# Kernel optimization log

Hardware: AMD Instinct MI355X
Metric: run time of the kernel (lower is better)

The kernel has to match this reference:

```python
import jax, jax.numpy as jnp
import numpy as np

B, S, H, E, V = 4, 256, 1024, 1024, 50257
PAD = 0
DOM = 0.9   # skipLayersDominance
EPS = 1e-5  # LayerNorm eps (torch default)


def setup_inputs() -> dict:
    key = jax.random.key(0)
    ks = jax.random.split(key, 6)
    emb = jax.random.normal(ks[0], (V, E), jnp.float32) * 0.02
    emb = emb.at[PAD].set(0.0)  # padding_idx row zeroed like nn.Embedding
    labels = jax.random.randint(ks[1], (B, S), 0, V)
    W_in = jax.random.normal(ks[2], (E, H), jnp.float32) * (1.0 / np.sqrt(E))
    b_in = jnp.zeros((H,), jnp.float32)
    # Conv1d(2H, H, kernel_size=1, groups=H) weight -> [H, 2] (per-head pair mix)
    W_sani = jax.random.normal(ks[3], (H, 2), jnp.float32) * (1.0 / np.sqrt(2.0))
    b_sani = jnp.zeros((H,), jnp.float32)
    ln_w = jnp.ones((H,), jnp.float32)
    ln_b = jnp.zeros((H,), jnp.float32)
    W_out = jax.random.normal(ks[4], (H, E), jnp.float32) * (1.0 / np.sqrt(H))
    b_out = jnp.zeros((E,), jnp.float32)
    return dict(labels=labels, emb=emb, W_in=W_in, b_in=b_in, W_sani=W_sani,
                b_sani=b_sani, ln_w=ln_w, ln_b=ln_b, W_out=W_out, b_out=b_out)


def _layernorm(x, w, b):
    mu = x.mean(-1, keepdims=True)
    var = x.var(-1, keepdims=True)
    return (x - mu) * jax.lax.rsqrt(var + EPS) * w + b


def _forward(labels, emb, W_in, b_in, W_sani, b_sani, ln_w, ln_b, W_out, b_out):
    x = emb[labels]                                # [B,S,E] inputsEmbeddings
    h = jax.nn.relu(x @ W_in + b_in)               # [B,S,H] inputState
    pos = jnp.arange(S)

    def step(hidden, L):
        # positions <= L are replaced by blank (zeros) per the torch cat logic
        mask = (pos > L)[None, :, None]
        shifted = jnp.concatenate([jnp.zeros_like(hidden[:, :1]), hidden[:, :-1]], axis=1)
        prev = jnp.where(mask, shifted, 0.0)       # hidden[t-1] for t>L else 0
        curr = jnp.where(mask, hidden, 0.0)        # hidden[t]   for t>L else 0
        # torch stack(dim=1)+reshape(B, 2H, 1) == concat(prev, curr) on features;
        # grouped conv (groups=H, 2 ch/group, k=1): out[g] = W[g,0]*cat[2g] + W[g,1]*cat[2g+1] + b[g]
        pair = jnp.concatenate([prev, curr], axis=-1).reshape(B, S, H, 2)
        out = jax.nn.relu(jnp.einsum('bshc,hc->bsh', pair, W_sani) + b_sani)
        out = out * (1.0 - DOM) + hidden           # skipLayers: + sequentialInputState
        out = _layernorm(out, ln_w, ln_b)           # skipLayersNorm
        return out, None

    h, _ = jax.lax.scan(jax.checkpoint(step), h, jnp.arange(S))
    y = jax.nn.relu(h @ W_out + b_out)             # [B,S,E]
    # torch CrossEntropyLoss with float (soft) targets: classes along dim=1 (S)
    logp = jax.nn.log_softmax(y, axis=1)
    loss = -(x * logp).sum(axis=1).mean()
    return loss


def reference(labels, emb, W_in, b_in, W_sani, b_sani, ln_w, ln_b, W_out, b_out):
    return _forward(labels, emb, W_in, b_in, W_sani, b_sani, ln_w, ln_b, W_out, b_out)
```

## Files before the change

### kernel.cpp

```cpp
#include <hip/hip_runtime.h>
#include <cstdint>

#define H_DIM 1024
#define S_LEN 256
#define NBLK_SCAN 128
#define GDEPTH 16
#define DOMC ((float)(1.0 - 0.9))
#define EPS_LN 1e-5f

typedef float v2f __attribute__((ext_vector_type(2)));

template <int CTRL, int RMASK, bool BC>
__device__ __forceinline__ float dpp_term(float x) {
    return __int_as_float(__builtin_amdgcn_update_dpp(
        0, __float_as_int(x), CTRL, RMASK, 0xf, BC));
}
__device__ __forceinline__ float wave_reduce_sum(float x) {
    x += dpp_term<0x111, 0xf, true>(x);
    x += dpp_term<0x112, 0xf, true>(x);
    x += dpp_term<0x114, 0xf, true>(x);
    x += dpp_term<0x118, 0xf, true>(x);
    x += dpp_term<0x142, 0xa, false>(x);
    x += dpp_term<0x143, 0xc, false>(x);
    return __int_as_float(__builtin_amdgcn_readlane(__float_as_int(x), 63));
}

__device__ __forceinline__ int llc_load_int(const int* p) {
    int v;
    asm volatile("global_load_dword %0, %1, off sc0 sc1\n\ts_waitcnt vmcnt(0)"
                 : "=v"(v) : "v"(p) : "memory");
    return v;
}
__device__ __forceinline__ void llc_store_int(int* p, int v) {
    asm volatile("global_store_dword %0, %1, off sc0 sc1" :: "v"(p), "v"(v)
                 : "memory");
}
__device__ __forceinline__ void llc_store_row_nowait(float* base, const float* h) {
    asm volatile(
        "global_store_dword %16, %0, off sc0 sc1\n\t"
        "global_store_dword %16, %1, off offset:256 sc0 sc1\n\t"
        "global_store_dword %16, %2, off offset:512 sc0 sc1\n\t"
        "global_store_dword %16, %3, off offset:768 sc0 sc1\n\t"
        "global_store_dword %16, %4, off offset:1024 sc0 sc1\n\t"
        "global_store_dword %16, %5, off offset:1280 sc0 sc1\n\t"
        "global_store_dword %16, %6, off offset:1536 sc0 sc1\n\t"
        "global_store_dword %16, %7, off offset:1792 sc0 sc1\n\t"
        "global_store_dword %16, %8, off offset:2048 sc0 sc1\n\t"
        "global_store_dword %16, %9, off offset:2304 sc0 sc1\n\t"
        "global_store_dword %16, %10, off offset:2560 sc0 sc1\n\t"
        "global_store_dword %16, %11, off offset:2816 sc0 sc1\n\t"
        "global_store_dword %16, %12, off offset:3072 sc0 sc1\n\t"
        "global_store_dword %16, %13, off offset:3328 sc0 sc1\n\t"
        "global_store_dword %16, %14, off offset:3584 sc0 sc1\n\t"
        "global_store_dword %16, %15, off offset:3840 sc0 sc1"
        :: "v"(h[0]), "v"(h[1]), "v"(h[2]), "v"(h[3]),
           "v"(h[4]), "v"(h[5]), "v"(h[6]), "v"(h[7]),
           "v"(h[8]), "v"(h[9]), "v"(h[10]), "v"(h[11]),
           "v"(h[12]), "v"(h[13]), "v"(h[14]), "v"(h[15]), "v"(base)
        : "memory");
}
__device__ __forceinline__ void llc_publish_lag2(float* dbase, int* flagp,
                                                 int flagval, const float* h) {
    asm volatile(
        "s_waitcnt vmcnt(16)\n\t"
        "global_store_dword %17, %18, off sc0 sc1\n\t"
        "global_store_dword %16, %0, off sc0 sc1\n\t"
        "global_store_dword %16, %1, off offset:256 sc0 sc1\n\t"
        "global_store_dword %16, %2, off offset:512 sc0 sc1\n\t"
        "global_store_dword %16, %3, off offset:768 sc0 sc1\n\t"
        "global_store_dword %16, %4, off offset:1024 sc0 sc1\n\t"
        "global_store_dword %16, %5, off offset:1280 sc0 sc1\n\t"
        "global_store_dword %16, %6, off offset:1536 sc0 sc1\n\t"
        "global_store_dword %16, %7, off offset:1792 sc0 sc1\n\t"
        "global_store_dword %16, %8, off offset:2048 sc0 sc1\n\t"
        "global_store_dword %16, %9, off offset:2304 sc0 sc1\n\t"
        "global_store_dword %16, %10, off offset:2560 sc0 sc1\n\t"
        "global_store_dword %16, %11, off offset:2816 sc0 sc1\n\t"
        "global_store_dword %16, %12, off offset:3072 sc0 sc1\n\t"
        "global_store_dword %16, %13, off offset:3328 sc0 sc1\n\t"
        "global_store_dword %16, %14, off offset:3584 sc0 sc1\n\t"
        "global_store_dword %16, %15, off offset:3840 sc0 sc1"
        :: "v"(h[0]), "v"(h[1]), "v"(h[2]), "v"(h[3]),
           "v"(h[4]), "v"(h[5]), "v"(h[6]), "v"(h[7]),
           "v"(h[8]), "v"(h[9]), "v"(h[10]), "v"(h[11]),
           "v"(h[12]), "v"(h[13]), "v"(h[14]), "v"(h[15]),
           "v"(dbase), "v"(flagp), "v"(flagval)
        : "memory");
}
__device__ __forceinline__ void llc_release(int* flagp, int flagval) {
    asm volatile("s_waitcnt vmcnt(0)\n\t"
                 "global_store_dword %0, %1, off sc0 sc1"
                 :: "v"(flagp), "v"(flagval) : "memory");
}

__device__ __forceinline__ void dma_slot(const float* gslot, float* stg, int l) {
#pragma unroll
    for (int c = 0; c < 4; ++c)
        __builtin_amdgcn_global_load_lds(
            (const __attribute__((address_space(1))) uint32_t*)(gslot + c * 256 + l * 4),
            (__attribute__((address_space(3))) uint32_t*)(stg + c * 256),
            16, 0, 0x11);
}

__device__ __forceinline__ void make_pairs(const float* hv, v2f* c7, int l) {
    const int s0 = (2 * l) & 63, s1 = (2 * l + 1) & 63;
    const bool hi = (l >= 32);
#pragma unroll
    for (int j = 0; j < 8; ++j) {
        float x0 = __shfl(hv[2 * j], s0, 64);
        float x1 = __shfl(hv[2 * j + 1], s0, 64);
        float y0 = __shfl(hv[2 * j], s1, 64);
        float y1 = __shfl(hv[2 * j + 1], s1, 64);
        c7[j].x = hi ? x1 : x0;
        c7[j].y = hi ? y1 : y0;
    }
}

template <bool GATHER>
__global__ __launch_bounds__(256) void gemm_relu_kernel(
    const float* __restrict__ A, const int* __restrict__ labels,
    const float* __restrict__ emb, const float* __restrict__ W,
    const float* __restrict__ bias, float* __restrict__ out)
{
    __shared__ float As[16][68];
    __shared__ float Bs[16][64];
    __shared__ int   lab[64];

    const int tid = threadIdx.x;
    const int bx = blockIdx.x & 15;
    const int by = blockIdx.x >> 4;
    const int m0 = by * 64, n0 = bx * 64;

    if (GATHER && tid < 64) lab[tid] = labels[m0 + tid];
    __syncthreads();

    const int tx = tid & 15, ty = tid >> 4;
    const int mload = tid >> 2;
    const int kq    = (tid & 3) * 4;
    const int kb    = tid >> 4;
    const int nb    = (tid & 15) * 4;

    const float* aBase;
    if (GATHER) aBase = emb + (size_t)lab[mload] * 1024 + kq;
    else        aBase = A   + (size_t)(m0 + mload) * 1024 + kq;
    const float* bBase = W + (size_t)kb * 1024 + n0 + nb;

    float4 a_pre = *(const float4*)aBase;
    float4 b_pre = *(const float4*)bBase;

    float acc[4][4] = {};

    for (int k0 = 0; k0 < 1024; k0 += 16) {
        As[kq + 0][mload] = a_pre.x;
        As[kq + 1][mload] = a_pre.y;
        As[kq + 2][mload] = a_pre.z;
        As[kq + 3][mload] = a_pre.w;
        *(float4*)&Bs[kb][nb] = b_pre;
        __syncthreads();

        if (k0 + 16 < 1024) {
            a_pre = *(const float4*)(aBase + k0 + 16);
            b_pre = *(const float4*)(bBase + (size_t)(k0 + 16) * 1024);
        }

#pragma unroll
        for (int kk = 0; kk < 16; ++kk) {
            float a_[4];
#pragma unroll
            for (int i = 0; i < 4; ++i) a_[i] = As[kk][ty * 4 + i];
            float4 bv = *(const float4*)&Bs[kk][tx * 4];
            float b_[4] = {bv.x, bv.y, bv.z, bv.w};
#pragma unroll
            for (int i = 0; i < 4; ++i)
#pragma unroll
                for (int j = 0; j < 4; ++j)
                    acc[i][j] = fmaf(a_[i], b_[j], acc[i][j]);
        }
        __syncthreads();
    }

    float bias4[4];
#pragma unroll
    for (int j = 0; j < 4; ++j) bias4[j] = bias[n0 + tx * 4 + j];
#pragma unroll
    for (int i = 0; i < 4; ++i) {
        float4 o;
        o.x = fmaxf(acc[i][0] + bias4[0], 0.f);
        o.y = fmaxf(acc[i][1] + bias4[1], 0.f);
        o.z = fmaxf(acc[i][2] + bias4[2], 0.f);
        o.w = fmaxf(acc[i][3] + bias4[3], 0.f);
        *(float4*)&out[(size_t)(m0 + ty * 4 + i) * 1024 + n0 + tx * 4] = o;
    }
}

__global__ __launch_bounds__(256) void scan_init_kernel(
    int* __restrict__ prodG, int* __restrict__ consG)
{
    const int tid = threadIdx.x;
    if (tid < NBLK_SCAN) { prodG[tid * 32] = -2; consG[tid * 32] = -2; }
}

__global__ __launch_bounds__(512, 1) void scan_kernel(
    const float* __restrict__ h0, float* __restrict__ hf,
    const float* __restrict__ Wsani, const float* __restrict__ bsani,
    const float* __restrict__ lnw, const float* __restrict__ lnb,
    float* __restrict__ gbuf, int* __restrict__ prodG, int* __restrict__ consG)
{
    __shared__ float ring[7][2][H_DIM];
    __shared__ float stg[H_DIM];
    __shared__ int prodL[8], consL[8];

    const int tid = threadIdx.x, w = tid >> 6, l = tid & 63;
    const int Bb = blockIdx.x;
    const int b = Bb >> 5, p = Bb & 31;
    const int t = 8 * p + w;
    const int row = b * S_LEN + t;
    const bool hasR = (p < 31);
    const int leftB = Bb - 1, rightB = Bb + 1;

    float w0c[16], w1c[16], bsc[16], lwc[16], lbc[16], hv[16];
#pragma unroll
    for (int i = 0; i < 16; ++i) {
        int h = l + 64 * i;
        w0c[i] = Wsani[2 * h]; w1c[i] = Wsani[2 * h + 1];
        bsc[i] = bsani[h]; lwc[i] = lnw[h]; lbc[i] = lnb[h];
        hv[i] = h0[(size_t)row * H_DIM + h];
    }

    if (tid < 8) { prodL[tid] = -2; consL[tid] = -2; }
    __syncthreads();

    v2f c7[8];
    if (w < 7) {
#pragma unroll
        for (int i = 0; i < 16; ++i) ring[w][1][l + 64 * i] = hv[i];
        __threadfence_block();
        if (l == 0) ((volatile int*)prodL)[w] = -1;
    } else {
        if (hasR)
            llc_store_row_nowait(
                gbuf + ((size_t)Bb * GDEPTH + (GDEPTH - 1)) * H_DIM + l, hv);
        make_pairs(hv, c7, l);
    }

    const float inv1024 = 1.f / 1024.f;
    int F = -2, pfL = -3, consCache = -2;
    float vv[16];

    for (int L = 0; L < S_LEN; ++L) {
        const bool active = (L < t);
        if (active) {
            v2f pv[8], cv[8];
            if (w == 0) {
                const int* fp = prodG + leftB * 32;
                if (pfL != L - 1) {
                    while (F < L - 1) {
                        F = llc_load_int(fp);
                        if (F < L - 1) __builtin_amdgcn_s_sleep(1);
                    }
                    dma_slot(gbuf + ((size_t)leftB * GDEPTH +
                                     ((L - 1) & (GDEPTH - 1))) * H_DIM, stg, l);
                    pfL = L - 1;
                }
                asm volatile("s_waitcnt vmcnt(0)" ::: "memory");
#pragma unroll
                for (int j = 0; j < 8; ++j)
                    pv[j] = *(const v2f*)&stg[2 * l + 128 * j];
#pragma unroll
                for (int j = 0; j < 8; ++j)
                    cv[j] = *(const v2f*)&ring[0][(L - 1) & 1][2 * l + 128 * j];
                if (F < L) F = llc_load_int(fp);
                if (F >= L && L < t - 1) {
                    asm volatile("s_waitcnt lgkmcnt(0)" ::: "memory");
                    dma_slot(gbuf + ((size_t)leftB * GDEPTH +
                                     (L & (GDEPTH - 1))) * H_DIM, stg, l);
                    pfL = L;
                }
                llc_store_int(consG + Bb * 32, L);
            } else {
                int spin = 0;
                while (((volatile int*)prodL)[w - 1] < L - 1)
                    { if (++spin > 8) __builtin_amdgcn_s_sleep(1); }
                const float* srcp = &ring[w - 1][(L - 1) & 1][0];
#pragma unroll
                for (int j = 0; j < 8; ++j)
                    pv[j] = *(const v2f*)&srcp[2 * l + 128 * j];
                if (w < 7) {
                    const float* srcc = &ring[w][(L - 1) & 1][0];
#pragma unroll
                    for (int j = 0; j < 8; ++j)
                        cv[j] = *(const v2f*)&srcc[2 * l + 128 * j];
                } else {
#pragma unroll
                    for (int j = 0; j < 8; ++j) cv[j] = c7[j];
                }
                if (l == 0) ((volatile int*)consL)[w] = L - 1;
            }
#pragma unroll
            for (int i = 0; i < 8; ++i) {
                float s = fmaf(pv[i].x, w0c[i], fmaf(pv[i].y, w1c[i], bsc[i]));
                s = fmaxf(s, 0.f);
                vv[i] = fmaf(DOMC, s, hv[i]);
            }
#pragma unroll
            for (int i = 8; i < 16; ++i) {
                float s = fmaf(cv[i - 8].x, w0c[i],
                               fmaf(cv[i - 8].y, w1c[i], bsc[i]));
                s = fmaxf(s, 0.f);
                vv[i] = fmaf(DOMC, s, hv[i]);
            }
        } else {
#pragma unroll
            for (int i = 0; i < 16; ++i) {
                float s = fmaxf(bsc[i], 0.f);
                vv[i] = fmaf(DOMC, s, hv[i]);
            }
        }
        float sum = 0.f, ss = 0.f;
#pragma unroll
        for (int i = 0; i < 16; ++i) { sum += vv[i]; ss = fmaf(vv[i], vv[i], ss); }
        sum = wave_reduce_sum(sum); ss = wave_reduce_sum(ss);
        const float mu = sum * inv1024;
        const float var = fmaf(-mu, mu, ss * inv1024);
        const float r = 1.f / sqrtf(var + EPS_LN);
#pragma unroll
        for (int i = 0; i < 16; ++i)
            hv[i] = fmaf((vv[i] - mu) * r, lwc[i], lbc[i]);

        if (active) {
            if (w < 7) {
                if (L >= 1) {
                    int spin = 0;
                    while (((volatile int*)consL)[w + 1] < L - 2)
                        { if (++spin > 8) __builtin_amdgcn_s_sleep(1); }
                }
#pragma unroll
                for (int i = 0; i < 16; ++i) ring[w][L & 1][l + 64 * i] = hv[i];
                __threadfence_block();
                if (l == 0) ((volatile int*)prodL)[w] = L;
            } else {
                if (hasR) {
                    if (consCache < L - (GDEPTH - 3)) {
                        int c = llc_load_int(consG + rightB * 32);
                        while (c < L - (GDEPTH - 1)) {
                            __builtin_amdgcn_s_sleep(1);
                            c = llc_load_int(consG + rightB * 32);
                        }
                        consCache = c;
                    }
                    llc_publish_lag2(
                        gbuf + ((size_t)Bb * GDEPTH + (L & (GDEPTH - 1))) * H_DIM + l,
                        prodG + Bb * 32, L - 2, hv);
                }
                if (L + 1 < t) make_pairs(hv, c7, l);
            }
        } else if (w == 7 && hasR && L == t) {
            llc_release(prodG + Bb * 32, t - 1);
        }
    }
#pragma unroll
    for (int i = 0; i < 16; ++i)
        hf[(size_t)row * H_DIM + l + 64 * i] = hv[i];
}

__global__ __launch_bounds__(256) void lse_kernel(
    const float* __restrict__ y, float* __restrict__ lse)
{
    const int b = blockIdx.x >> 4, et = blockIdx.x & 15;
    const int col = threadIdx.x & 63, rg = threadIdx.x >> 6;
    const int e = et * 64 + col;
    const float* yb = y + (size_t)b * S_LEN * H_DIM + e;
    float m = -INFINITY, s = 0.f;
    for (int r = rg; r < S_LEN; r += 4) {
        float v = yb[(size_t)r * H_DIM];
        float mn = fmaxf(m, v);
        s = fmaf(s, expf(m - mn), expf(v - mn));
        m = mn;
    }
    __shared__ float sm[4][64], sp[4][64];
    sm[rg][col] = m; sp[rg][col] = s;
    __syncthreads();
    if (threadIdx.x < 64) {
        const int c = threadIdx.x;
        float M = fmaxf(fmaxf(sm[0][c], sm[1][c]), fmaxf(sm[2][c], sm[3][c]));
        float S = sp[0][c] * expf(sm[0][c] - M) + sp[1][c] * expf(sm[1][c] - M)
                + sp[2][c] * expf(sm[2][c] - M) + sp[3][c] * expf(sm[3][c] - M);
        lse[b * H_DIM + et * 64 + c] = M + logf(S);
    }
}

__global__ __launch_bounds__(256) void loss_row_kernel(
    const float* __restrict__ y, const int* __restrict__ labels,
    const float* __restrict__ emb, const float* __restrict__ lse,
    float* __restrict__ partials)
{
    const int bs = blockIdx.x;
    const int b = bs >> 8;
    const int lab = labels[bs];
    const float* yr = y + (size_t)bs * H_DIM;
    const float* er = emb + (size_t)lab * H_DIM;
    const float* lr = lse + b * H_DIM;
    float acc = 0.f;
#pragma unroll
    for (int i = 0; i < 4; ++i) {
        int e = threadIdx.x + 256 * i;
        acc = fmaf(er[e], yr[e] - lr[e], acc);
    }
    acc = wave_reduce_sum(acc);
    __shared__ float wsum[4];
    if ((threadIdx.x & 63) == 0) wsum[threadIdx.x >> 6] = acc;
    __syncthreads();
    if (threadIdx.x == 0)
        partials[bs] = (wsum[0] + wsum[1]) + (wsum[2] + wsum[3]);
}

__global__ __launch_bounds__(256) void loss_final_kernel(
    const float* __restrict__ partials, float* __restrict__ out)
{
    const int tid = threadIdx.x;
    float a = 0.f;
#pragma unroll
    for (int j = 0; j < 4; ++j) a += partials[tid + 256 * j];
    a = wave_reduce_sum(a);
    __shared__ float wsum[4];
    if ((tid & 63) == 0) wsum[tid >> 6] = a;
    __syncthreads();
    if (tid == 0)
        out[0] = -((wsum[0] + wsum[1]) + (wsum[2] + wsum[3])) * (1.f / 4096.f);
}

extern "C" void kernel_launch(void* const* d_in, const int* in_sizes, int n_in,
                              void* d_out, int out_size, void* d_ws, size_t ws_size,
                              hipStream_t stream)
{
    const int*   labels = (const int*)  d_in[0];
    const float* emb    = (const float*)d_in[1];
    const float* W_in   = (const float*)d_in[2];
    const float* b_in   = (const float*)d_in[3];
    const float* W_sani = (const float*)d_in[4];
    const float* b_sani = (const float*)d_in[5];
    const float* ln_w   = (const float*)d_in[6];
    const float* ln_b   = (const float*)d_in[7];
    const float* W_out  = (const float*)d_in[8];
    const float* b_out  = (const float*)d_in[9];
    float* out = (float*)d_out;

    float* ws = (float*)d_ws;
    float* h0       = ws;
    float* hf       = ws + (1 << 20);
    float* yb       = ws + 2 * (1 << 20);
    float* gbuf     = ws + 3 * (1 << 20);
    float* lse      = ws + 5 * (1 << 20);
    float* partials = lse + 4096;
    int*   prodG    = (int*)(partials + 1024);
    int*   consG    = prodG + NBLK_SCAN * 32;

    gemm_relu_kernel<true><<<dim3(256), dim3(256), 0, stream>>>(
        nullptr, labels, emb, W_in, b_in, h0);
    scan_init_kernel<<<dim3(1), dim3(256), 0, stream>>>(prodG, consG);
    {
        const float* a_h0 = h0; float* a_hf = hf;
        const float* a_ws = W_sani; const float* a_bs = b_sani;
        const float* a_lw = ln_w;   const float* a_lb = ln_b;
        float* a_gb = gbuf; int* a_pf = prodG; int* a_cf = consG;
        void* args[] = { (void*)&a_h0, (void*)&a_hf, (void*)&a_ws, (void*)&a_bs,
                         (void*)&a_lw, (void*)&a_lb, (void*)&a_gb,
                         (void*)&a_pf, (void*)&a_cf };
        hipLaunchCooperativeKernel((const void*)scan_kernel,
                                   dim3(NBLK_SCAN), dim3(512), args, 0, stream);
    }
    gemm_relu_kernel<false><<<dim3(256), dim3(256), 0, stream>>>(
        hf, nullptr, emb, W_out, b_out, yb);
    lse_kernel<<<dim3(64), dim3(256), 0, stream>>>(yb, lse);
    loss_row_kernel<<<dim3(1024), dim3(256), 0, stream>>>(
        yb, labels, emb, lse, partials);
    loss_final_kernel<<<dim3(1), dim3(256), 0, stream>>>(partials, out);
}
```

Before: 748.7 us.

## Cut inter-block handoff latency in scan with lag-1 flags and async flag prefetch

Changes the cross-block producer/consumer protocol in the sequential scan. The producer now publishes its flag with lag 1 instead of lag 2, issued right after the 16 data stores. The consumer double-buffers the LDS staging slot and prefetches the producer flag into LDS via global_load_lds, so the next slot's DMA can start earlier and the consumer flag is posted sooner. The separate init kernel is folded into the first GEMM to save one launch. This shortens the critical path between neighbouring blocks but makes the memory-ordering reasoning more fragile, since the release now relies on a vmcnt wait inside the store sequence.

Measured after the change: 728.3 us. 1.03x faster.

```diff
diff --git a/kernel.cpp b/kernel.cpp
--- a/kernel.cpp
+++ b/kernel.cpp
@@ -59,11 +59,9 @@
            "v"(h[12]), "v"(h[13]), "v"(h[14]), "v"(h[15]), "v"(base)
         : "memory");
 }
-__device__ __forceinline__ void llc_publish_lag2(float* dbase, int* flagp,
+__device__ __forceinline__ void llc_publish_lag1(float* dbase, int* flagp,
                                                  int flagval, const float* h) {
     asm volatile(
-        "s_waitcnt vmcnt(16)\n\t"
-        "global_store_dword %17, %18, off sc0 sc1\n\t"
         "global_store_dword %16, %0, off sc0 sc1\n\t"
         "global_store_dword %16, %1, off offset:256 sc0 sc1\n\t"
         "global_store_dword %16, %2, off offset:512 sc0 sc1\n\t"
@@ -79,7 +77,9 @@
         "global_store_dword %16, %12, off offset:3072 sc0 sc1\n\t"
         "global_store_dword %16, %13, off offset:3328 sc0 sc1\n\t"
         "global_store_dword %16, %14, off offset:3584 sc0 sc1\n\t"
-        "global_store_dword %16, %15, off offset:3840 sc0 sc1"
+        "global_store_dword %16, %15, off offset:3840 sc0 sc1\n\t"
+        "s_waitcnt vmcnt(16)\n\t"
+        "global_store_dword %17, %18, off sc0 sc1"
         :: "v"(h[0]), "v"(h[1]), "v"(h[2]), "v"(h[3]),
            "v"(h[4]), "v"(h[5]), "v"(h[6]), "v"(h[7]),
            "v"(h[8]), "v"(h[9]), "v"(h[10]), "v"(h[11]),
@@ -100,6 +100,11 @@
             (const __attribute__((address_space(1))) uint32_t*)(gslot + c * 256 + l * 4),
             (__attribute__((address_space(3))) uint32_t*)(stg + c * 256),
             16, 0, 0x11);
+}
+__device__ __forceinline__ void flag_dma(const int* fp, int* stgf) {
+    __builtin_amdgcn_global_load_lds(
+        (const __attribute__((address_space(1))) uint32_t*)fp,
+        (__attribute__((address_space(3))) uint32_t*)stgf, 4, 0, 0x11);
 }
 
 __device__ __forceinline__ void make_pairs(const float* hv, v2f* c7, int l) {
@@ -120,7 +125,8 @@
 __global__ __launch_bounds__(256) void gemm_relu_kernel(
     const float* __restrict__ A, const int* __restrict__ labels,
     const float* __restrict__ emb, const float* __restrict__ W,
-    const float* __restrict__ bias, float* __restrict__ out)
+    const float* __restrict__ bias, float* __restrict__ out,
+    int* __restrict__ prodG, int* __restrict__ consG)
 {
     __shared__ float As[16][68];
     __shared__ float Bs[16][64];
@@ -131,6 +137,10 @@
     const int by = blockIdx.x >> 4;
     const int m0 = by * 64, n0 = bx * 64;
 
+    if (GATHER && blockIdx.x == 0) {
+        if (tid < NBLK_SCAN) prodG[tid * 32] = -2;
+        else                 consG[(tid - NBLK_SCAN) * 32] = -2;
+    }
     if (GATHER && tid < 64) lab[tid] = labels[m0 + tid];
     __syncthreads();
 
@@ -193,13 +203,6 @@
     }
 }
 
-__global__ __launch_bounds__(256) void scan_init_kernel(
-    int* __restrict__ prodG, int* __restrict__ consG)
-{
-    const int tid = threadIdx.x;
-    if (tid < NBLK_SCAN) { prodG[tid * 32] = -2; consG[tid * 32] = -2; }
-}
-
 __global__ __launch_bounds__(512, 1) void scan_kernel(
     const float* __restrict__ h0, float* __restrict__ hf,
     const float* __restrict__ Wsani, const float* __restrict__ bsani,
@@ -207,7 +210,8 @@
     float* __restrict__ gbuf, int* __restrict__ prodG, int* __restrict__ consG)
 {
     __shared__ float ring[7][2][H_DIM];
-    __shared__ float stg[H_DIM];
+    __shared__ float stg[2][H_DIM];
+    __shared__ int   stgflag[64];
     __shared__ int prodL[8], consL[8];
 
     const int tid = threadIdx.x, w = tid >> 6, l = tid & 63;
@@ -227,7 +231,8 @@
         hv[i] = h0[(size_t)row * H_DIM + h];
     }
 
-    if (tid < 8) { prodL[tid] = -2; consL[tid] = -2; }
+    if (tid < 8)  { prodL[tid] = -2; consL[tid] = -2; }
+    if (tid < 64) stgflag[tid] = -2;
     __syncthreads();
 
     v2f c7[8];
@@ -253,30 +258,39 @@
             v2f pv[8], cv[8];
             if (w == 0) {
                 const int* fp = prodG + leftB * 32;
+                asm volatile("s_waitcnt vmcnt(0)" ::: "memory");
+                {
+                    int fa = ((volatile int*)stgflag)[0];
+                    if (fa > F) F = fa;
+                }
                 if (pfL != L - 1) {
                     while (F < L - 1) {
-                        F = llc_load_int(fp);
+                        F = __builtin_amdgcn_readfirstlane(llc_load_int(fp));
                         if (F < L - 1) __builtin_amdgcn_s_sleep(1);
                     }
                     dma_slot(gbuf + ((size_t)leftB * GDEPTH +
-                                     ((L - 1) & (GDEPTH - 1))) * H_DIM, stg, l);
+                                     ((L - 1) & (GDEPTH - 1))) * H_DIM,
+                             stg[(L - 1) & 1], l);
                     pfL = L - 1;
-                }
-                asm volatile("s_waitcnt vmcnt(0)" ::: "memory");
+                    asm volatile("s_waitcnt vmcnt(0)" ::: "memory");
+                }
+                llc_store_int(consG + Bb * 32, L);
+                const float* srcp = stg[(L - 1) & 1];
 #pragma unroll
                 for (int j = 0; j < 8; ++j)
-                    pv[j] = *(const v2f*)&stg[2 * l + 128 * j];
+                    pv[j] = *(const v2f*)&srcp[2 * l + 128 * j];
 #pragma unroll
                 for (int j = 0; j < 8; ++j)
                     cv[j] = *(const v2f*)&ring[0][(L - 1) & 1][2 * l + 128 * j];
-                if (F < L) F = llc_load_int(fp);
-                if (F >= L && L < t - 1) {
-                    asm volatile("s_waitcnt lgkmcnt(0)" ::: "memory");
-                    dma_slot(gbuf + ((size_t)leftB * GDEPTH +
-                                     (L & (GDEPTH - 1))) * H_DIM, stg, l);
-                    pfL = L;
-                }
-                llc_store_int(consG + Bb * 32, L);
+                if (L < t - 1) {
+                    if (F >= L) {
+                        dma_slot(gbuf + ((size_t)leftB * GDEPTH +
+                                         (L & (GDEPTH - 1))) * H_DIM,
+                                 stg[L & 1], l);
+                        pfL = L;
+                    }
+                    flag_dma(fp, stgflag);
+                }
             } else {
                 int spin = 0;
                 while (((volatile int*)prodL)[w - 1] < L - 1)
@@ -346,11 +360,11 @@
                             __builtin_amdgcn_s_sleep(1);
                             c = llc_load_int(consG + rightB * 32);
                         }
-                        consCache = c;
+                        consCache = __builtin_amdgcn_readfirstlane(c);
                     }
-                    llc_publish_lag2(
+                    llc_publish_lag1(
                         gbuf + ((size_t)Bb * GDEPTH + (L & (GDEPTH - 1))) * H_DIM + l,
-                        prodG + Bb * 32, L - 2, hv);
+                        prodG + Bb * 32, L - 1, hv);
                 }
                 if (L + 1 < t) make_pairs(hv, c7, l);
             }
@@ -456,8 +470,7 @@
     int*   consG    = prodG + NBLK_SCAN * 32;
 
     gemm_relu_kernel<true><<<dim3(256), dim3(256), 0, stream>>>(
-        nullptr, labels, emb, W_in, b_in, h0);
-    scan_init_kernel<<<dim3(1), dim3(256), 0, stream>>>(prodG, consG);
+        nullptr, labels, emb, W_in, b_in, h0, prodG, consG);
     {
         const float* a_h0 = h0; float* a_hf = hf;
         const float* a_ws = W_sani; const float* a_bs = b_sani;
@@ -470,7 +483,7 @@
                                    dim3(NBLK_SCAN), dim3(512), args, 0, stream);
     }
     gemm_relu_kernel<false><<<dim3(256), dim3(256), 0, stream>>>(
-        hf, nullptr, emb, W_out, b_out, yb);
+        hf, nullptr, emb, W_out, b_out, yb, nullptr, nullptr);
     lse_kernel<<<dim3(64), dim3(256), 0, stream>>>(yb, lse);
     loss_row_kernel<<<dim3(1024), dim3(256), 0, stream>>>(
         yb, labels, emb, lse, partials);
```
